# Performance work log

Hardware: AMD Instinct MI355X
Metric: run time of the kernel (lower is better)

Reference implementation:

```python
import jax, jax.numpy as jnp
import numpy as np

EMB = 1024
HEADS = 16
HEAD_DIM = EMB // HEADS
DIM_FF = 4096
EPS = 1e-05


def layer_norm(x, gain, bias):
    # BasicLayerNorm: (x - mean) / (std + eps), std with unbiased=False
    mean = jnp.mean(x, axis=-1, keepdims=True)
    std = jnp.sqrt(jnp.mean((x - mean) ** 2, axis=-1, keepdims=True))
    return gain * ((x - mean) / (std + EPS)) + bias


def setup_inputs() -> dict:
    key = jax.random.key(0)
    ks = jax.random.split(key, 8)
    scale = 1.0 / np.sqrt(EMB)
    x = jax.random.normal(ks[0], (4, 2048, EMB), dtype=jnp.float32)
    Wq = jax.random.normal(ks[1], (EMB, EMB), dtype=jnp.float32) * scale
    Wk = jax.random.normal(ks[2], (EMB, EMB), dtype=jnp.float32) * scale
    Wv = jax.random.normal(ks[3], (EMB, EMB), dtype=jnp.float32) * scale
    Wo = jax.random.normal(ks[4], (EMB, EMB), dtype=jnp.float32) * scale
    W1 = jax.random.normal(ks[5], (EMB, DIM_FF), dtype=jnp.float32) * scale
    b1 = jnp.zeros((DIM_FF,), dtype=jnp.float32)
    W2 = jax.random.normal(ks[6], (DIM_FF, EMB), dtype=jnp.float32) * (1.0 / np.sqrt(DIM_FF))
    b2 = jnp.zeros((EMB,), dtype=jnp.float32)
    gain1 = jnp.ones((EMB,), dtype=jnp.float32)
    bias1 = jnp.zeros((EMB,), dtype=jnp.float32)
    gain2 = jnp.ones((EMB,), dtype=jnp.float32)
    bias2 = jnp.zeros((EMB,), dtype=jnp.float32)
    return dict(x=x, Wq=Wq, Wk=Wk, Wv=Wv, Wo=Wo, W1=W1, b1=b1, W2=W2, b2=b2,
                gain1=gain1, bias1=bias1, gain2=gain2, bias2=bias2)


def reference(x, Wq, Wk, Wv, Wo, W1, b1, W2, b2, gain1, bias1, gain2, bias2):
    b, t, e = x.shape
    h, dk = HEADS, HEAD_DIM
    # QKV projections, split heads -> (b, h, t, dk)
    q = (x @ Wq).reshape(b, t, h, dk).transpose(0, 2, 1, 3)
    k = (x @ Wk).reshape(b, t, h, dk).transpose(0, 2, 1, 3)
    v = (x @ Wv).reshape(b, t, h, dk).transpose(0, 2, 1, 3)
    # scaled dot-product attention
    scores = jnp.einsum('bhqd,bhkd->bhqk', q, k) / jnp.sqrt(jnp.float32(dk))
    attn = jax.nn.softmax(scores, axis=-1)
    ctx = jnp.einsum('bhqk,bhkd->bhqd', attn, v)
    # merge heads and output projection
    merged = ctx.transpose(0, 2, 1, 3).reshape(b, t, e)
    attended = merged @ Wo
    # residual + layer norm 1 (dropout is identity at inference)
    x1 = layer_norm(attended + x, gain1, bias1)
    # feed-forward
    ff = jax.nn.relu(x1 @ W1 + b1) @ W2 + b2
    # residual + layer norm 2
    return layer_norm(ff + x1, gain2, bias2)
```

## Files before the change

### kernel.cpp

```cpp
#include <hip/hip_runtime.h>
#include <hip/hip_bf16.h>
#include <math.h>

#define EMB 1024
#define DIM_FF 4096
#define HEADS 16
#define HD 64
#define TSEQ 2048
#define BATCH 4
#define MROWS (BATCH*TSEQ)
#define LN_EPS 1e-5f

typedef __attribute__((ext_vector_type(8))) short short8;
typedef __attribute__((ext_vector_type(4))) float f32x4;

#define MFMA16(a,b,c) __builtin_amdgcn_mfma_f32_16x16x32_bf16((a),(b),(c),0,0,0)

#define GLOBAL_AS(p) ((const __attribute__((address_space(1))) void*)(p))
#define LDS_AS(p)    ((__attribute__((address_space(3))) void*)(p))

__device__ __forceinline__ unsigned short bf16bits(float f){
    __hip_bfloat16 h = __float2bfloat16(f);
    unsigned short u;
    __builtin_memcpy(&u, &h, 2);
    return u;
}

__global__ __launch_bounds__(256)
void cvt_bf16(const float* __restrict__ in, __hip_bfloat16* __restrict__ out, int n4){
    int i = blockIdx.x*256 + threadIdx.x;
    if (i >= n4) return;
    f32x4 v = reinterpret_cast<const f32x4*>(in)[i];
    union { unsigned short us[4]; uint2 u2; } o;
    #pragma unroll
    for (int j=0;j<4;++j) o.us[j] = bf16bits(v[j]);
    *reinterpret_cast<uint2*>(reinterpret_cast<unsigned short*>(out) + (size_t)i*4) = o.u2;
}

__global__ __launch_bounds__(256)
void transpose_cvt(const float* __restrict__ in, __hip_bfloat16* __restrict__ out, int R, int C){
    __shared__ __hip_bfloat16 tile[32][33];
    int bx = blockIdx.x*32;
    int by = blockIdx.y*32;
    int x = bx + threadIdx.x;
    #pragma unroll
    for (int i = threadIdx.y; i < 32; i += 8){
        tile[i][threadIdx.x] = __float2bfloat16(in[(size_t)(by+i)*C + x]);
    }
    __syncthreads();
    int xo = by + threadIdx.x;
    #pragma unroll
    for (int i = threadIdx.y; i < 32; i += 8){
        out[(size_t)(bx+i)*R + xo] = tile[threadIdx.x][i];
    }
}

template<int EPI>
__global__ __launch_bounds__(256, 2)
void gemm_bt(const __hip_bfloat16* __restrict__ A,
             const __hip_bfloat16* __restrict__ Bt,
             int M, int N, int K,
             float* __restrict__ Cf,
             const float* __restrict__ bias)
{
    __shared__ __align__(16) __hip_bfloat16 As[128*32];
    __shared__ __align__(16) __hip_bfloat16 Bs[128*32];
    const int tid = threadIdx.x;
    const int lane = tid & 63;
    const int wid = tid >> 6;
    const int wm = wid >> 1, wn = wid & 1;
    const int row0 = blockIdx.x * 128;
    const int col0 = blockIdx.y * 128;
    const int rA = lane & 15, kg = lane >> 4;

    const int lrow = lane >> 2;
    const int lcol = (lane & 3) << 3;

    f32x4 acc[4][4] = {};

    for (int kt = 0; kt < K; kt += 32) {
        __syncthreads();
        #pragma unroll
        for (int half = 0; half < 2; ++half) {
            const int rbase = (wid << 5) + (half << 4);
            const int r = rbase + lrow;
            __builtin_amdgcn_global_load_lds(
                GLOBAL_AS(A + (size_t)(row0 + r)*K + kt + lcol),
                LDS_AS(&As[rbase*32]), 16, 0, 0);
            __builtin_amdgcn_global_load_lds(
                GLOBAL_AS(Bt + (size_t)(col0 + r)*K + kt + lcol),
                LDS_AS(&Bs[rbase*32]), 16, 0, 0);
        }
        __syncthreads();
        short8 af[4], bfr[4];
        #pragma unroll
        for (int mi = 0; mi < 4; ++mi)
            af[mi] = *reinterpret_cast<const short8*>(&As[(wm*64 + mi*16 + rA)*32 + (kg<<3)]);
        #pragma unroll
        for (int ni = 0; ni < 4; ++ni)
            bfr[ni] = *reinterpret_cast<const short8*>(&Bs[(wn*64 + ni*16 + rA)*32 + (kg<<3)]);
        #pragma unroll
        for (int mi = 0; mi < 4; ++mi)
            #pragma unroll
            for (int ni = 0; ni < 4; ++ni)
                acc[mi][ni] = MFMA16(af[mi], bfr[ni], acc[mi][ni]);
    }

    #pragma unroll
    for (int mi=0; mi<4; ++mi) {
        #pragma unroll
        for (int ni=0; ni<4; ++ni) {
            #pragma unroll
            for (int j=0;j<4;++j){
                float v = acc[mi][ni][j];
                int grow = row0 + wm*64 + mi*16 + (kg<<2) + j;
                int gcol = col0 + wn*64 + ni*16 + rA;
                if constexpr (EPI==1) {
                    Cf[(size_t)grow*N + gcol] = v;
                } else {
                    Cf[(size_t)grow*N + gcol] = v + bias[gcol];
                }
            }
        }
    }
}

#define GPHASE(P, STAGE_EXPR, WAIT_EXPR) do { \
    short8 af[2][2]; \
    _Pragma("unroll") \
    for (int i_=0;i_<2;++i_){ \
      _Pragma("unroll") \
      for (int kk_=0;kk_<2;++kk_) \
        af[i_][kk_] = *reinterpret_cast<const short8*>(pA + ((2*(P)+i_)*16+rA)*128 + (((kk_<<2)+kg)^swz)*16); \
    } \
    STAGE_EXPR; WAIT_EXPR; \
    __builtin_amdgcn_s_barrier(); \
    __builtin_amdgcn_s_setprio(1); \
    _Pragma("unroll") \
    for (int i_=0;i_<2;++i_){ \
      _Pragma("unroll") \
      for (int ni_=0;ni_<4;++ni_){ \
        acc[2*(P)+i_][ni_] = MFMA16(af[i_][0], bfr[ni_][0], acc[2*(P)+i_][ni_]); \
        acc[2*(P)+i_][ni_] = MFMA16(af[i_][1], bfr[ni_][1], acc[2*(P)+i_][ni_]); \
      } \
    } \
    __builtin_amdgcn_s_setprio(0); \
    __builtin_amdgcn_s_barrier(); \
} while(0)

template<int EPI>
__global__ __launch_bounds__(512, 2)
void gemm256(const __hip_bfloat16* __restrict__ A,
             const __hip_bfloat16* __restrict__ Bt,
             int M, int N, int K,
             __hip_bfloat16* __restrict__ Cb,
             const float* __restrict__ bias,
             __hip_bfloat16* __restrict__ qo,
             __hip_bfloat16* __restrict__ ko,
             __hip_bfloat16* __restrict__ vto)
{
    __shared__ __align__(16) __hip_bfloat16 Al[2][16384];
    __shared__ __align__(16) __hip_bfloat16 Bl[2][16384];
    const int tid = threadIdx.x;
    const int lane = tid & 63;
    const int wid = tid >> 6;
    const int wm = wid >> 2, wn = wid & 3;
    const int row0 = blockIdx.x * 256;
    const int col0 = blockIdx.y * 256;
    const int rA = lane & 15, kg = lane >> 4, swz = rA & 7;
    const int NT = K >> 6;

    const int lr = lane >> 3;
    const int lg = (lane & 7) ^ lr;
    const __hip_bfloat16* sA = A  + (size_t)(row0 + wid*8 + lr)*K + lg*8;
    const __hip_bfloat16* sB = Bt + (size_t)(col0 + wid*8 + lr)*K + lg*8;
    char* dA = (char*)&Al[0][0] + wid*8*128;
    char* dB = (char*)&Bl[0][0] + wid*8*128;

    auto stage = [&](const __hip_bfloat16* s, char* d, int buf, int half, int kt){
        #pragma unroll
        for (int rr = 0; rr < 2; ++rr)
            __builtin_amdgcn_global_load_lds(
                GLOBAL_AS(s + (size_t)(half*128 + rr*64)*K + kt),
                LDS_AS(d + buf*32768 + (half*128 + rr*64)*128), 16, 0, 0);
    };

    f32x4 acc[8][4] = {};

    stage(sA, dA, 0, 0, 0); stage(sA, dA, 0, 1, 0);
    stage(sB, dB, 0, 0, 0); stage(sB, dB, 0, 1, 0);
    stage(sB, dB, 1, 0, 64); stage(sB, dB, 1, 1, 64);
    asm volatile("s_waitcnt vmcnt(4)" ::: "memory");
    __builtin_amdgcn_sched_barrier(0);
    __builtin_amdgcn_s_barrier();

    const char* cA = (const char*)&Al[0][0] + wm*128*128;
    const char* cB = (const char*)&Bl[0][0] + wn*64*128;

    for (int t = 0; t < NT; ++t) {
        const int buf = t & 1;
        const char* pA = cA + buf*32768;
        const char* pB = cB + buf*32768;
        short8 bfr[4][2];
        #pragma unroll
        for (int ni = 0; ni < 4; ++ni)
            #pragma unroll
            for (int kk = 0; kk < 2; ++kk)
                bfr[ni][kk] = *reinterpret_cast<const short8*>(pB + (ni*16+rA)*128 + (((kk<<2)+kg)^swz)*16);

        GPHASE(0, if (t+1 < NT) stage(sA, dA, buf^1, 0, (t+1)*64), );
        GPHASE(1, if (t+1 < NT) stage(sA, dA, buf^1, 1, (t+1)*64), );
        GPHASE(2, if (t+2 < NT) stage(sB, dB, buf,   0, (t+2)*64), );
        GPHASE(3, if (t+2 < NT) stage(sB, dB, buf,   1, (t+2)*64),
            if (t+2 < NT) { asm volatile("s_waitcnt vmcnt(4)" ::: "memory"); }
            else          { asm volatile("s_waitcnt vmcnt(0)" ::: "memory"); }
            __builtin_amdgcn_sched_barrier(0) );
    }

    #pragma unroll
    for (int mi=0; mi<8; ++mi) {
        #pragma unroll
        for (int ni=0; ni<4; ++ni) {
            #pragma unroll
            for (int j=0;j<4;++j){
                float v = acc[mi][ni][j];
                int grow = row0 + wm*128 + mi*16 + (kg<<2) + j;
                int gcol = col0 + wn*64 + ni*16 + rA;
                if constexpr (EPI==0) {
                    int b = grow >> 11, t = grow & 2047;
                    int which = gcol >> 10, hdx = gcol & 1023;
                    int h = hdx >> 6, d = hdx & 63;
                    int bh = b*HEADS + h;
                    __hip_bfloat16 bv = __float2bfloat16(v);
                    if (which==0)      qo[((size_t)bh*TSEQ + t)*HD + d] = bv;
                    else if (which==1) ko[((size_t)bh*TSEQ + t)*HD + d] = bv;
                    else               vto[((size_t)bh*HD + d)*TSEQ + t] = bv;
                } else {
                    v += bias[gcol]; v = v > 0.0f ? v : 0.0f;
                    Cb[(size_t)grow*N + gcol] = __float2bfloat16(v);
                }
            }
        }
    }
}

__global__ __launch_bounds__(256, 4)
void attn_fwd(const __hip_bfloat16* __restrict__ q,
              const __hip_bfloat16* __restrict__ k,
              const __hip_bfloat16* __restrict__ vt,
              __hip_bfloat16* __restrict__ merged)
{
    const int wg = (blockIdx.x & 7) * 256 + (blockIdx.x >> 3);
    const int bh = wg >> 5;
    const int qt = wg & 31;
    const int wid = threadIdx.x >> 6, lane = threadIdx.x & 63;
    const int rA = lane & 15, kg = lane >> 4;
    const int qrow0 = qt*64 + wid*16;
    const __hip_bfloat16* Qh = q  + (size_t)bh*TSEQ*HD;
    const __hip_bfloat16* Kh = k  + (size_t)bh*TSEQ*HD;
    const __hip_bfloat16* Vh = vt + (size_t)bh*HD*TSEQ;

    __shared__ __align__(16) __hip_bfloat16 Kl[2][64*64];
    __shared__ __align__(16) __hip_bfloat16 Vl[2][64*64];
    __shared__ __align__(16) __hip_bfloat16 plds[4][8][16][8];

    short8 aQ0 = *reinterpret_cast<const short8*>(Qh + (size_t)(qrow0+rA)*HD + (kg<<3));
    short8 aQ1 = *reinterpret_cast<const short8*>(Qh + (size_t)(qrow0+rA)*HD + 32 + (kg<<3));

    const int lrow = lane >> 3;
    const int lslot = ((lane & 7) ^ lrow) << 3;
    const __hip_bfloat16* sK0 = Kh + (size_t)(wid*16 + lrow)*HD + lslot;
    const __hip_bfloat16* sV0 = Vh + (size_t)(wid*16 + lrow)*TSEQ + lslot;
    const int dOff = wid*16*64;

    f32x4 O[4] = {};
    float m = -1e30f, l = 0.f;
    const int swz = rA & 7;

    {
        __builtin_amdgcn_global_load_lds(GLOBAL_AS(sK0),          LDS_AS(&Kl[0][dOff]),        16, 0, 0);
        __builtin_amdgcn_global_load_lds(GLOBAL_AS(sK0 + 8*HD),   LDS_AS(&Kl[0][dOff + 8*64]), 16, 0, 0);
        __builtin_amdgcn_global_load_lds(GLOBAL_AS(sV0),          LDS_AS(&Vl[0][dOff]),        16, 0, 0);
        __builtin_amdgcn_global_load_lds(GLOBAL_AS(sV0 + 8*TSEQ), LDS_AS(&Vl[0][dOff + 8*64]), 16, 0, 0);
    }
    __syncthreads();

    for (int t = 0; t < TSEQ/64; ++t) {
        const int b = t & 1;
        if (t < TSEQ/64 - 1) {
            const int kt = (t+1)*64;
            __builtin_amdgcn_global_load_lds(GLOBAL_AS(sK0 + (size_t)kt*HD),          LDS_AS(&Kl[b^1][dOff]),        16, 0, 0);
            __builtin_amdgcn_global_load_lds(GLOBAL_AS(sK0 + (size_t)(kt+8)*HD),      LDS_AS(&Kl[b^1][dOff + 8*64]), 16, 0, 0);
            __builtin_amdgcn_global_load_lds(GLOBAL_AS(sV0 + kt),                     LDS_AS(&Vl[b^1][dOff]),        16, 0, 0);
            __builtin_amdgcn_global_load_lds(GLOBAL_AS(sV0 + 8*TSEQ + kt),            LDS_AS(&Vl[b^1][dOff + 8*64]), 16, 0, 0);
        }
        const char* Kb = (const char*)&Kl[b][0];
        const char* Vb = (const char*)&Vl[b][0];

        f32x4 st[4];
        #pragma unroll
        for (int kb = 0; kb < 4; ++kb) {
            const int ro = (kb*16 + rA) * 128;
            short8 aK0 = *reinterpret_cast<const short8*>(Kb + ro + ((kg ^ swz) << 4));
            short8 aK1 = *reinterpret_cast<const short8*>(Kb + ro + (((4+kg) ^ swz) << 4));
            f32x4 z = {};
            z = MFMA16(aK0, aQ0, z);
            st[kb] = MFMA16(aK1, aQ1, z);
        }
        f32x4 sm01, sm;
        #pragma unroll
        for (int j=0;j<4;++j) sm01[j] = fmaxf(st[0][j], st[1][j]);
        #pragma unroll
        for (int j=0;j<4;++j) sm[j] = fmaxf(sm01[j], fmaxf(st[2][j], st[3][j]));
        float mx = fmaxf(fmaxf(sm[0], sm[1]), fmaxf(sm[2], sm[3]));
        mx = fmaxf(mx, __shfl_xor(mx, 16));
        mx = fmaxf(mx, __shfl_xor(mx, 32));
        float mn = fmaxf(m, mx*0.125f);
        float al = __expf(m - mn);
        f32x4 ps[4];
        #pragma unroll
        for (int kb=0; kb<4; ++kb)
            #pragma unroll
            for (int j=0;j<4;++j)
                ps[kb][j] = __expf(fmaf(st[kb][j], 0.125f, -mn));
        f32x4 ssv = (ps[0]+ps[1]) + (ps[2]+ps[3]);
        float rs = (ssv[0]+ssv[1]) + (ssv[2]+ssv[3]);
        rs += __shfl_xor(rs, 16);
        rs += __shfl_xor(rs, 32);
        l = l*al + rs; m = mn;
        float alq[4];
        #pragma unroll
        for (int j=0;j<4;++j) alq[j] = __shfl(al, (kg<<2)+j);
        #pragma unroll
        for (int dt=0; dt<4; ++dt)
            #pragma unroll
            for (int j=0;j<4;++j) O[dt][j] *= alq[j];
        #pragma unroll
        for (int kb=0; kb<4; ++kb) {
            uint2 w;
            w.x = (unsigned)bf16bits(ps[kb][0]) | ((unsigned)bf16bits(ps[kb][1]) << 16);
            w.y = (unsigned)bf16bits(ps[kb][2]) | ((unsigned)bf16bits(ps[kb][3]) << 16);
            *reinterpret_cast<uint2*>(&plds[wid][2*kb + (kg>>1)][rA][(kg&1)<<2]) = w;
        }
        short8 aP0 = *reinterpret_cast<const short8*>(&plds[wid][kg][rA][0]);
        short8 aP1 = *reinterpret_cast<const short8*>(&plds[wid][4+kg][rA][0]);
        #pragma unroll
        for (int dt=0; dt<4; ++dt) {
            const int vo = (dt*16 + rA) * 128;
            short8 bV0 = *reinterpret_cast<const short8*>(Vb + vo + ((kg ^ swz) << 4));
            short8 bV1 = *reinterpret_cast<const short8*>(Vb + vo + (((4+kg) ^ swz) << 4));
            O[dt] = MFMA16(aP0, bV0, O[dt]);
            O[dt] = MFMA16(aP1, bV1, O[dt]);
        }
        __syncthreads();
    }

    float lq[4];
    #pragma unroll
    for (int j=0;j<4;++j) lq[j] = 1.0f / __shfl(l, (kg<<2)+j);
    const int b = bh >> 4, h = bh & 15;
    #pragma unroll
    for (int dt=0; dt<4; ++dt){
        #pragma unroll
        for (int j=0;j<4;++j){
            int t = qrow0 + (kg<<2) + j;
            int col = h*HD + dt*16 + rA;
            merged[((size_t)(b*TSEQ + t))*EMB + col] = __float2bfloat16(O[dt][j]*lq[j]);
        }
    }
}

__global__ __launch_bounds__(256)
void ln_res(const float* __restrict__ a, const float* __restrict__ res,
            const float* __restrict__ gain, const float* __restrict__ bias,
            float* __restrict__ outf, __hip_bfloat16* __restrict__ outb)
{
    const int row = blockIdx.x;
    const int tid = threadIdx.x;
    const int lane = tid & 63, wid = tid >> 6;
    const size_t base = (size_t)row * EMB;
    f32x4 va = *reinterpret_cast<const f32x4*>(a + base + tid*4);
    f32x4 vr = *reinterpret_cast<const f32x4*>(res + base + tid*4);
    f32x4 v = va + vr;
    float s = v[0]+v[1]+v[2]+v[3];
    #pragma unroll
    for (int off=1; off<64; off<<=1) s += __shfl_xor(s, off);
    __shared__ float red1[4], red2[4];
    if (lane==0) red1[wid] = s;
    __syncthreads();
    float mean = (red1[0]+red1[1]+red1[2]+red1[3]) * (1.0f/EMB);
    f32x4 d;
    #pragma unroll
    for (int j=0;j<4;++j) d[j] = v[j] - mean;
    float qs = d[0]*d[0]+d[1]*d[1]+d[2]*d[2]+d[3]*d[3];
    #pragma unroll
    for (int off=1; off<64; off<<=1) qs += __shfl_xor(qs, off);
    if (lane==0) red2[wid] = qs;
    __syncthreads();
    float var = (red2[0]+red2[1]+red2[2]+red2[3]) * (1.0f/EMB);
    float r = 1.0f/(sqrtf(var)+LN_EPS);
    f32x4 g = *reinterpret_cast<const f32x4*>(gain + tid*4);
    f32x4 bb = *reinterpret_cast<const f32x4*>(bias + tid*4);
    f32x4 o;
    #pragma unroll
    for (int j=0;j<4;++j) o[j] = g[j]*(d[j]*r) + bb[j];
    *reinterpret_cast<f32x4*>(outf + base + tid*4) = o;
    if (outb) {
        union { unsigned short us[4]; uint2 u2; } ob;
        #pragma unroll
        for (int j=0;j<4;++j) ob.us[j] = bf16bits(o[j]);
        *reinterpret_cast<uint2*>(reinterpret_cast<unsigned short*>(outb) + base + tid*4) = ob.u2;
    }
}

extern "C" void kernel_launch(void* const* d_in, const int* in_sizes, int n_in,
                              void* d_out, int out_size, void* d_ws, size_t ws_size,
                              hipStream_t stream) {
    const float* x   = (const float*)d_in[0];
    const float* Wq  = (const float*)d_in[1];
    const float* Wk  = (const float*)d_in[2];
    const float* Wv  = (const float*)d_in[3];
    const float* Wo  = (const float*)d_in[4];
    const float* W1  = (const float*)d_in[5];
    const float* b1  = (const float*)d_in[6];
    const float* W2  = (const float*)d_in[7];
    const float* b2  = (const float*)d_in[8];
    const float* gain1 = (const float*)d_in[9];
    const float* bias1 = (const float*)d_in[10];
    const float* gain2 = (const float*)d_in[11];
    const float* bias2 = (const float*)d_in[12];

    char* ws = (char*)d_ws;
    __hip_bfloat16* Wqkv_t = (__hip_bfloat16*)(ws + 0);
    __hip_bfloat16* Wo_t   = (__hip_bfloat16*)(ws + 6291456);
    __hip_bfloat16* W1_t   = (__hip_bfloat16*)(ws + 8388608);
    __hip_bfloat16* W2_t   = (__hip_bfloat16*)(ws + 16777216);
    __hip_bfloat16* xb     = (__hip_bfloat16*)(ws + 25165824);
    __hip_bfloat16* qb     = (__hip_bfloat16*)(ws + 41943040);
    __hip_bfloat16* kb     = (__hip_bfloat16*)(ws + 58720256);
    __hip_bfloat16* vtb    = (__hip_bfloat16*)(ws + 75497472);
    __hip_bfloat16* h1     = (__hip_bfloat16*)(ws + 25165824);
    __hip_bfloat16* mergedb= (__hip_bfloat16*)(ws + 92274688);
    float*          attended=(float*)(ws + 109051904);
    float*          ff     = (float*)(ws + 92274688);
    float*          x1f    = (float*)(ws + 142606336);
    __hip_bfloat16* x1b    = (__hip_bfloat16*)(ws + 176160768);
    float*          outf   = (float*)d_out;

    dim3 tb(32,8);
    transpose_cvt<<<dim3(32,32),  tb, 0, stream>>>(Wq, Wqkv_t,                 1024, 1024);
    transpose_cvt<<<dim3(32,32),  tb, 0, stream>>>(Wk, Wqkv_t + 1024*1024,     1024, 1024);
    transpose_cvt<<<dim3(32,32),  tb, 0, stream>>>(Wv, Wqkv_t + 2*1024*1024,   1024, 1024);
    transpose_cvt<<<dim3(32,32),  tb, 0, stream>>>(Wo, Wo_t,                   1024, 1024);
    transpose_cvt<<<dim3(128,32), tb, 0, stream>>>(W1, W1_t,                   1024, 4096);
    transpose_cvt<<<dim3(32,128), tb, 0, stream>>>(W2, W2_t,                   4096, 1024);
    cvt_bf16<<<(MROWS*EMB/4 + 255)/256, 256, 0, stream>>>(x, xb, MROWS*EMB/4);

    gemm256<0><<<dim3(MROWS/256, 3072/256), 512, 0, stream>>>(
        xb, Wqkv_t, MROWS, 3072, EMB, nullptr, nullptr, qb, kb, vtb);
    attn_fwd<<<dim3(2048), 256, 0, stream>>>(qb, kb, vtb, mergedb);
    gemm_bt<1><<<dim3(MROWS/128, EMB/128), 256, 0, stream>>>(
        mergedb, Wo_t, MROWS, EMB, EMB, attended, nullptr);
    ln_res<<<MROWS, 256, 0, stream>>>(attended, x, gain1, bias1, x1f, x1b);
    gemm256<2><<<dim3(MROWS/256, DIM_FF/256), 512, 0, stream>>>(
        x1b, W1_t, MROWS, DIM_FF, EMB, h1, b1, nullptr, nullptr, nullptr);
    gemm_bt<3><<<dim3(MROWS/128, EMB/128), 256, 0, stream>>>(
        h1, W2_t, MROWS, EMB, DIM_FF, ff, b2);
    ln_res<<<MROWS, 256, 0, stream>>>(ff, x1f, gain2, bias2, outf, nullptr);
}
```

Measured before the change: 487.7 us.

## Store intermediates in bf16, lazy softmax rescale, merge weight transposes, packed bf16 converts

The Wo and W2 GEMM outputs and the x1 residual now go to memory as bf16 instead of fp32, which roughly halves traffic into the layer-norm kernels. The fp32 copy of x1 is dropped. In attention the 1/sqrt(dk) scale is folded into Q in the QKV epilogue, and the online-softmax rescale is skipped unless the running max grows by more than 8. The row-sum reduction is also deferred to the end of the loop. Four weight-transpose launches are merged into one, and bf16 conversions use the packed v_cvt_pk_bf16_f32 instruction; the bf16 residual loses precision against the fp32 reference.

```diff
diff --git a/kernel.cpp b/kernel.cpp
--- a/kernel.cpp
+++ b/kernel.cpp
@@ -25,34 +25,62 @@
     __builtin_memcpy(&u, &h, 2);
     return u;
 }
+__device__ __forceinline__ unsigned cvtpk_bf16(float lo, float hi){
+    unsigned r;
+    asm("v_cvt_pk_bf16_f32 %0, %1, %2" : "=v"(r) : "v"(lo), "v"(hi));
+    return r;
+}
+__device__ __forceinline__ f32x4 ld4bf(const __hip_bfloat16* p){
+    ushort4 u = *reinterpret_cast<const ushort4*>(p);
+    union{unsigned i; float f;} c0,c1,c2,c3;
+    c0.i=(unsigned)u.x<<16; c1.i=(unsigned)u.y<<16; c2.i=(unsigned)u.z<<16; c3.i=(unsigned)u.w<<16;
+    f32x4 r; r[0]=c0.f; r[1]=c1.f; r[2]=c2.f; r[3]=c3.f;
+    return r;
+}
 
 __global__ __launch_bounds__(256)
 void cvt_bf16(const float* __restrict__ in, __hip_bfloat16* __restrict__ out, int n4){
     int i = blockIdx.x*256 + threadIdx.x;
     if (i >= n4) return;
     f32x4 v = reinterpret_cast<const f32x4*>(in)[i];
-    union { unsigned short us[4]; uint2 u2; } o;
-    #pragma unroll
-    for (int j=0;j<4;++j) o.us[j] = bf16bits(v[j]);
-    *reinterpret_cast<uint2*>(reinterpret_cast<unsigned short*>(out) + (size_t)i*4) = o.u2;
+    uint2 o;
+    o.x = cvtpk_bf16(v[0], v[1]);
+    o.y = cvtpk_bf16(v[2], v[3]);
+    *reinterpret_cast<uint2*>(reinterpret_cast<unsigned short*>(out) + (size_t)i*4) = o;
+}
+
+__global__ __launch_bounds__(256)
+void transpose_cvt4(const float* __restrict__ s0, const float* __restrict__ s1,
+                    const float* __restrict__ s2, const float* __restrict__ s3,
+                    __hip_bfloat16* __restrict__ out){
+    const float* in = blockIdx.z==0 ? s0 : blockIdx.z==1 ? s1 : blockIdx.z==2 ? s2 : s3;
+    __hip_bfloat16* dst = out + (size_t)blockIdx.z*1024*1024;
+    __shared__ __hip_bfloat16 tile[32][33];
+    int bx = blockIdx.x*32, by = blockIdx.y*32;
+    int x = bx + threadIdx.x;
+    #pragma unroll
+    for (int i = threadIdx.y; i < 32; i += 8)
+        tile[i][threadIdx.x] = __float2bfloat16(in[(size_t)(by+i)*1024 + x]);
+    __syncthreads();
+    int xo = by + threadIdx.x;
+    #pragma unroll
+    for (int i = threadIdx.y; i < 32; i += 8)
+        dst[(size_t)(bx+i)*1024 + xo] = tile[threadIdx.x][i];
 }
 
 __global__ __launch_bounds__(256)
 void transpose_cvt(const float* __restrict__ in, __hip_bfloat16* __restrict__ out, int R, int C){
     __shared__ __hip_bfloat16 tile[32][33];
-    int bx = blockIdx.x*32;
-    int by = blockIdx.y*32;
+    int bx = blockIdx.x*32, by = blockIdx.y*32;
     int x = bx + threadIdx.x;
     #pragma unroll
-    for (int i = threadIdx.y; i < 32; i += 8){
+    for (int i = threadIdx.y; i < 32; i += 8)
         tile[i][threadIdx.x] = __float2bfloat16(in[(size_t)(by+i)*C + x]);
-    }
     __syncthreads();
     int xo = by + threadIdx.x;
     #pragma unroll
-    for (int i = threadIdx.y; i < 32; i += 8){
+    for (int i = threadIdx.y; i < 32; i += 8)
         out[(size_t)(bx+i)*R + xo] = tile[threadIdx.x][i];
-    }
 }
 
 template<int EPI>
@@ -60,7 +88,7 @@
 void gemm_bt(const __hip_bfloat16* __restrict__ A,
              const __hip_bfloat16* __restrict__ Bt,
              int M, int N, int K,
-             float* __restrict__ Cf,
+             __hip_bfloat16* __restrict__ Cb,
              const float* __restrict__ bias)
 {
     __shared__ __align__(16) __hip_bfloat16 As[128*32];
@@ -115,11 +143,8 @@
                 float v = acc[mi][ni][j];
                 int grow = row0 + wm*64 + mi*16 + (kg<<2) + j;
                 int gcol = col0 + wn*64 + ni*16 + rA;
-                if constexpr (EPI==1) {
-                    Cf[(size_t)grow*N + gcol] = v;
-                } else {
-                    Cf[(size_t)grow*N + gcol] = v + bias[gcol];
-                }
+                if constexpr (EPI==3) v += bias[gcol];
+                Cb[(size_t)grow*N + gcol] = __float2bfloat16(v);
             }
         }
     }
@@ -231,10 +256,9 @@
                     int which = gcol >> 10, hdx = gcol & 1023;
                     int h = hdx >> 6, d = hdx & 63;
                     int bh = b*HEADS + h;
-                    __hip_bfloat16 bv = __float2bfloat16(v);
-                    if (which==0)      qo[((size_t)bh*TSEQ + t)*HD + d] = bv;
-                    else if (which==1) ko[((size_t)bh*TSEQ + t)*HD + d] = bv;
-                    else               vto[((size_t)bh*HD + d)*TSEQ + t] = bv;
+                    if (which==0)      qo[((size_t)bh*TSEQ + t)*HD + d] = __float2bfloat16(v*0.125f);
+                    else if (which==1) ko[((size_t)bh*TSEQ + t)*HD + d] = __float2bfloat16(v);
+                    else               vto[((size_t)bh*HD + d)*TSEQ + t] = __float2bfloat16(v);
                 } else {
                     v += bias[gcol]; v = v > 0.0f ? v : 0.0f;
                     Cb[(size_t)grow*N + gcol] = __float2bfloat16(v);
@@ -274,7 +298,7 @@
     const int dOff = wid*16*64;
 
     f32x4 O[4] = {};
-    float m = -1e30f, l = 0.f;
+    float m = -1e30f, lpart = 0.f;
     const int swz = rA & 7;
 
     {
@@ -289,10 +313,10 @@
         const int b = t & 1;
         if (t < TSEQ/64 - 1) {
             const int kt = (t+1)*64;
-            __builtin_amdgcn_global_load_lds(GLOBAL_AS(sK0 + (size_t)kt*HD),          LDS_AS(&Kl[b^1][dOff]),        16, 0, 0);
-            __builtin_amdgcn_global_load_lds(GLOBAL_AS(sK0 + (size_t)(kt+8)*HD),      LDS_AS(&Kl[b^1][dOff + 8*64]), 16, 0, 0);
-            __builtin_amdgcn_global_load_lds(GLOBAL_AS(sV0 + kt),                     LDS_AS(&Vl[b^1][dOff]),        16, 0, 0);
-            __builtin_amdgcn_global_load_lds(GLOBAL_AS(sV0 + 8*TSEQ + kt),            LDS_AS(&Vl[b^1][dOff + 8*64]), 16, 0, 0);
+            __builtin_amdgcn_global_load_lds(GLOBAL_AS(sK0 + (size_t)kt*HD),     LDS_AS(&Kl[b^1][dOff]),        16, 0, 0);
+            __builtin_amdgcn_global_load_lds(GLOBAL_AS(sK0 + (size_t)(kt+8)*HD), LDS_AS(&Kl[b^1][dOff + 8*64]), 16, 0, 0);
+            __builtin_amdgcn_global_load_lds(GLOBAL_AS(sV0 + kt),                LDS_AS(&Vl[b^1][dOff]),        16, 0, 0);
+            __builtin_amdgcn_global_load_lds(GLOBAL_AS(sV0 + 8*TSEQ + kt),       LDS_AS(&Vl[b^1][dOff + 8*64]), 16, 0, 0);
         }
         const char* Kb = (const char*)&Kl[b][0];
         const char* Vb = (const char*)&Vl[b][0];
@@ -307,39 +331,40 @@
             z = MFMA16(aK0, aQ0, z);
             st[kb] = MFMA16(aK1, aQ1, z);
         }
-        f32x4 sm01, sm;
-        #pragma unroll
-        for (int j=0;j<4;++j) sm01[j] = fmaxf(st[0][j], st[1][j]);
-        #pragma unroll
-        for (int j=0;j<4;++j) sm[j] = fmaxf(sm01[j], fmaxf(st[2][j], st[3][j]));
-        float mx = fmaxf(fmaxf(sm[0], sm[1]), fmaxf(sm[2], sm[3]));
+        f32x4 m4 = st[0];
+        #pragma unroll
+        for (int kb=1; kb<4; ++kb)
+            #pragma unroll
+            for (int j=0;j<4;++j) m4[j] = fmaxf(m4[j], st[kb][j]);
+        float mx = fmaxf(fmaxf(m4[0], m4[1]), fmaxf(m4[2], m4[3]));
         mx = fmaxf(mx, __shfl_xor(mx, 16));
         mx = fmaxf(mx, __shfl_xor(mx, 32));
-        float mn = fmaxf(m, mx*0.125f);
-        float al = __expf(m - mn);
+        if (!__all(mx - m <= 8.0f)) {
+            float mn = fmaxf(m, mx);
+            float al = __expf(m - mn);
+            lpart *= al;
+            float alq[4];
+            #pragma unroll
+            for (int j=0;j<4;++j) alq[j] = __shfl(al, (kg<<2)+j);
+            #pragma unroll
+            for (int dt=0; dt<4; ++dt)
+                #pragma unroll
+                for (int j=0;j<4;++j) O[dt][j] *= alq[j];
+            m = mn;
+        }
         f32x4 ps[4];
         #pragma unroll
         for (int kb=0; kb<4; ++kb)
             #pragma unroll
             for (int j=0;j<4;++j)
-                ps[kb][j] = __expf(fmaf(st[kb][j], 0.125f, -mn));
+                ps[kb][j] = __expf(st[kb][j] - m);
         f32x4 ssv = (ps[0]+ps[1]) + (ps[2]+ps[3]);
-        float rs = (ssv[0]+ssv[1]) + (ssv[2]+ssv[3]);
-        rs += __shfl_xor(rs, 16);
-        rs += __shfl_xor(rs, 32);
-        l = l*al + rs; m = mn;
-        float alq[4];
-        #pragma unroll
-        for (int j=0;j<4;++j) alq[j] = __shfl(al, (kg<<2)+j);
-        #pragma unroll
-        for (int dt=0; dt<4; ++dt)
-            #pragma unroll
-            for (int j=0;j<4;++j) O[dt][j] *= alq[j];
+        lpart += (ssv[0]+ssv[1]) + (ssv[2]+ssv[3]);
         #pragma unroll
         for (int kb=0; kb<4; ++kb) {
             uint2 w;
-            w.x = (unsigned)bf16bits(ps[kb][0]) | ((unsigned)bf16bits(ps[kb][1]) << 16);
-            w.y = (unsigned)bf16bits(ps[kb][2]) | ((unsigned)bf16bits(ps[kb][3]) << 16);
+            w.x = cvtpk_bf16(ps[kb][0], ps[kb][1]);
+            w.y = cvtpk_bf16(ps[kb][2], ps[kb][3]);
             *reinterpret_cast<uint2*>(&plds[wid][2*kb + (kg>>1)][rA][(kg&1)<<2]) = w;
         }
         short8 aP0 = *reinterpret_cast<const short8*>(&plds[wid][kg][rA][0]);
@@ -355,9 +380,12 @@
         __syncthreads();
     }
 
+    float lrow_ = lpart;
+    lrow_ += __shfl_xor(lrow_, 16);
+    lrow_ += __shfl_xor(lrow_, 32);
     float lq[4];
     #pragma unroll
-    for (int j=0;j<4;++j) lq[j] = 1.0f / __shfl(l, (kg<<2)+j);
+    for (int j=0;j<4;++j) lq[j] = 1.0f / __shfl(lrow_, (kg<<2)+j);
     const int b = bh >> 4, h = bh & 15;
     #pragma unroll
     for (int dt=0; dt<4; ++dt){
@@ -370,8 +398,9 @@
     }
 }
 
+template<int ABF, int RBF>
 __global__ __launch_bounds__(256)
-void ln_res(const float* __restrict__ a, const float* __restrict__ res,
+void ln_res(const void* __restrict__ a_, const void* __restrict__ res_,
             const float* __restrict__ gain, const float* __restrict__ bias,
             float* __restrict__ outf, __hip_bfloat16* __restrict__ outb)
 {
@@ -379,8 +408,11 @@
     const int tid = threadIdx.x;
     const int lane = tid & 63, wid = tid >> 6;
     const size_t base = (size_t)row * EMB;
-    f32x4 va = *reinterpret_cast<const f32x4*>(a + base + tid*4);
-    f32x4 vr = *reinterpret_cast<const f32x4*>(res + base + tid*4);
+    f32x4 va, vr;
+    if constexpr (ABF) va = ld4bf((const __hip_bfloat16*)a_ + base + tid*4);
+    else               va = *reinterpret_cast<const f32x4*>((const float*)a_ + base + tid*4);
+    if constexpr (RBF) vr = ld4bf((const __hip_bfloat16*)res_ + base + tid*4);
+    else               vr = *reinterpret_cast<const f32x4*>((const float*)res_ + base + tid*4);
     f32x4 v = va + vr;
     float s = v[0]+v[1]+v[2]+v[3];
     #pragma unroll
@@ -404,12 +436,13 @@
     f32x4 o;
     #pragma unroll
     for (int j=0;j<4;++j) o[j] = g[j]*(d[j]*r) + bb[j];
-    *reinterpret_cast<f32x4*>(outf + base + tid*4) = o;
+    if (outf)
+        *reinterpret_cast<f32x4*>(outf + base + tid*4) = o;
     if (outb) {
-        union { unsigned short us[4]; uint2 u2; } ob;
-        #pragma unroll
-        for (int j=0;j<4;++j) ob.us[j] = bf16bits(o[j]);
-        *reinterpret_cast<uint2*>(reinterpret_cast<unsigned short*>(outb) + base + tid*4) = ob.u2;
+        uint2 ob;
+        ob.x = cvtpk_bf16(o[0], o[1]);
+        ob.y = cvtpk_bf16(o[2], o[3]);
+        *reinterpret_cast<uint2*>(reinterpret_cast<unsigned short*>(outb) + base + tid*4) = ob;
     }
 }
 
@@ -431,40 +464,36 @@
     const float* bias2 = (const float*)d_in[12];
 
     char* ws = (char*)d_ws;
-    __hip_bfloat16* Wqkv_t = (__hip_bfloat16*)(ws + 0);
-    __hip_bfloat16* Wo_t   = (__hip_bfloat16*)(ws + 6291456);
-    __hip_bfloat16* W1_t   = (__hip_bfloat16*)(ws + 8388608);
-    __hip_bfloat16* W2_t   = (__hip_bfloat16*)(ws + 16777216);
-    __hip_bfloat16* xb     = (__hip_bfloat16*)(ws + 25165824);
-    __hip_bfloat16* qb     = (__hip_bfloat16*)(ws + 41943040);
-    __hip_bfloat16* kb     = (__hip_bfloat16*)(ws + 58720256);
-    __hip_bfloat16* vtb    = (__hip_bfloat16*)(ws + 75497472);
-    __hip_bfloat16* h1     = (__hip_bfloat16*)(ws + 25165824);
-    __hip_bfloat16* mergedb= (__hip_bfloat16*)(ws + 92274688);
-    float*          attended=(float*)(ws + 109051904);
-    float*          ff     = (float*)(ws + 92274688);
-    float*          x1f    = (float*)(ws + 142606336);
-    __hip_bfloat16* x1b    = (__hip_bfloat16*)(ws + 176160768);
-    float*          outf   = (float*)d_out;
+    __hip_bfloat16* Wqkv_t   = (__hip_bfloat16*)(ws + 0);
+    __hip_bfloat16* Wo_t     = (__hip_bfloat16*)(ws + 6291456);
+    __hip_bfloat16* W1_t     = (__hip_bfloat16*)(ws + 8388608);
+    __hip_bfloat16* W2_t     = (__hip_bfloat16*)(ws + 16777216);
+    __hip_bfloat16* xb       = (__hip_bfloat16*)(ws + 25165824);
+    __hip_bfloat16* qb       = (__hip_bfloat16*)(ws + 41943040);
+    __hip_bfloat16* kbuf     = (__hip_bfloat16*)(ws + 58720256);
+    __hip_bfloat16* vtb      = (__hip_bfloat16*)(ws + 75497472);
+    __hip_bfloat16* h1       = (__hip_bfloat16*)(ws + 25165824);
+    __hip_bfloat16* mergedb  = (__hip_bfloat16*)(ws + 92274688);
+    __hip_bfloat16* ffb      = (__hip_bfloat16*)(ws + 92274688);
+    __hip_bfloat16* attendedb= (__hip_bfloat16*)(ws + 109051904);
+    __hip_bfloat16* x1b      = (__hip_bfloat16*)(ws + 125829120);
+    float*          outf     = (float*)d_out;
 
     dim3 tb(32,8);
-    transpose_cvt<<<dim3(32,32),  tb, 0, stream>>>(Wq, Wqkv_t,                 1024, 1024);
-    transpose_cvt<<<dim3(32,32),  tb, 0, stream>>>(Wk, Wqkv_t + 1024*1024,     1024, 1024);
-    transpose_cvt<<<dim3(32,32),  tb, 0, stream>>>(Wv, Wqkv_t + 2*1024*1024,   1024, 1024);
-    transpose_cvt<<<dim3(32,32),  tb, 0, stream>>>(Wo, Wo_t,                   1024, 1024);
-    transpose_cvt<<<dim3(128,32), tb, 0, stream>>>(W1, W1_t,                   1024, 4096);
-    transpose_cvt<<<dim3(32,128), tb, 0, stream>>>(W2, W2_t,                   4096, 1024);
+    transpose_cvt4<<<dim3(32,32,4), tb, 0, stream>>>(Wq, Wk, Wv, Wo, Wqkv_t);
+    transpose_cvt<<<dim3(128,32), tb, 0, stream>>>(W1, W1_t, 1024, 4096);
+    transpose_cvt<<<dim3(32,128), tb, 0, stream>>>(W2, W2_t, 4096, 1024);
     cvt_bf16<<<(MROWS*EMB/4 + 255)/256, 256, 0, stream>>>(x, xb, MROWS*EMB/4);
 
     gemm256<0><<<dim3(MROWS/256, 3072/256), 512, 0, stream>>>(
-        xb, Wqkv_t, MROWS, 3072, EMB, nullptr, nullptr, qb, kb, vtb);
-    attn_fwd<<<dim3(2048), 256, 0, stream>>>(qb, kb, vtb, mergedb);
+        xb, Wqkv_t, MROWS, 3072, EMB, nullptr, nullptr, qb, kbuf, vtb);
+    attn_fwd<<<dim3(2048), 256, 0, stream>>>(qb, kbuf, vtb, mergedb);
     gemm_bt<1><<<dim3(MROWS/128, EMB/128), 256, 0, stream>>>(
-        mergedb, Wo_t, MROWS, EMB, EMB, attended, nullptr);
-    ln_res<<<MROWS, 256, 0, stream>>>(attended, x, gain1, bias1, x1f, x1b);
+        mergedb, Wo_t, MROWS, EMB, EMB, attendedb, nullptr);
+    ln_res<1,0><<<MROWS, 256, 0, stream>>>(attendedb, x, gain1, bias1, nullptr, x1b);
     gemm256<2><<<dim3(MROWS/256, DIM_FF/256), 512, 0, stream>>>(
         x1b, W1_t, MROWS, DIM_FF, EMB, h1, b1, nullptr, nullptr, nullptr);
     gemm_bt<3><<<dim3(MROWS/128, EMB/128), 256, 0, stream>>>(
-        h1, W2_t, MROWS, EMB, DIM_FF, ff, b2);
-    ln_res<<<MROWS, 256, 0, stream>>>(ff, x1f, gain2, bias2, outf, nullptr);
-}
+        h1, W2_t, MROWS, EMB, DIM_FF, ffb, b2);
+    ln_res<1,1><<<MROWS, 256, 0, stream>>>(ffb, x1b, gain2, bias2, outf, nullptr);
+}
```

Measured after the change: 442.6 us. 1.1x faster.
